# Performance work log

Hardware: AMD Instinct MI355X
Metric: run time of the kernel (lower is better)

## Reference

```python
import jax, jax.numpy as jnp
import numpy as np

DIM = 1024
HEADS = 16
DH = DIM // HEADS          # 64
ROT_DIM = 2 * DH           # 128, rotary applied over concatenated x/a head dim
B, N = 2, 2048


def l2norm(t, eps=1e-12):
    # F.normalize(p=2, dim=-1)
    n = jnp.sqrt(jnp.sum(t * t, axis=-1, keepdims=True))
    return t / jnp.maximum(n, eps)


def rotate_half(t):
    t1, t2 = jnp.split(t, 2, axis=-1)
    return jnp.concatenate([-t2, t1], axis=-1)


def apply_rotary(q, k):
    # q: [b,h,n,ROT_DIM], k: [b,1,n,ROT_DIM]
    n = q.shape[-2]
    inv_freq = 1.0 / (10000.0 ** (jnp.arange(0, ROT_DIM, 2, dtype=jnp.float32) / ROT_DIM))
    freqs = jnp.outer(jnp.arange(n, dtype=jnp.float32), inv_freq)  # [n, ROT_DIM/2]
    emb = jnp.concatenate([freqs, freqs], axis=-1)                 # [n, ROT_DIM]
    cos, sin = jnp.cos(emb), jnp.sin(emb)
    q = q * cos + rotate_half(q) * sin
    k = k * cos + rotate_half(k) * sin
    return q, k


def setup_inputs() -> dict:
    key = jax.random.key(0)
    ks = jax.random.split(key, 6)
    s = 0.02
    return {
        "x": jax.random.normal(ks[0], (B, N, DIM), jnp.float32),
        "a": jax.random.normal(ks[1], (B, N, DIM), jnp.float32),
        "Wq_x": jax.random.normal(ks[2], (DIM, DIM), jnp.float32) * s,
        "Wkv_x": jax.random.normal(ks[3], (2 * DH, DIM), jnp.float32) * s,
        "Wq_a": jax.random.normal(ks[4], (DIM, DIM), jnp.float32) * s,
        "Wkv_a": jax.random.normal(ks[5], (2 * DH, DIM), jnp.float32) * s,
        "qx_scale": jnp.ones((HEADS, 1, DH), jnp.float32),
        "qa_scale": jnp.ones((HEADS, 1, DH), jnp.float32),
        "kx_scale": jnp.ones((1, 1, DH), jnp.float32),
        "ka_scale": jnp.ones((1, 1, DH), jnp.float32),
    }


def reference(x, a, Wq_x, Wkv_x, Wq_a, Wkv_a, qx_scale, qa_scale, kx_scale, ka_scale):
    b, n, _ = x.shape
    # q projections: [b,n,dim] -> [b,h,n,dh]
    q_x = (x @ Wq_x.T).reshape(b, n, HEADS, DH).transpose(0, 2, 1, 3)
    q_a = (a @ Wq_a.T).reshape(b, n, HEADS, DH).transpose(0, 2, 1, 3)
    # shared single KV head: [b,n,2*dh] -> two [b,1,n,dh]
    kv_x = x @ Wkv_x.T
    k_x, v_x = jnp.split(kv_x[:, None], 2, axis=-1)
    kv_a = a @ Wkv_a.T
    k_a, v_a = jnp.split(kv_a[:, None], 2, axis=-1)
    # qk-norm with learned per-head (q) / shared (k) scales
    q_x = l2norm(q_x) * qx_scale
    q_a = l2norm(q_a) * qa_scale
    k_x = l2norm(k_x) * kx_scale
    k_a = l2norm(k_a) * ka_scale
    # concat modalities along feature dim -> head dim 2*dh
    q = jnp.concatenate([q_x, q_a], axis=-1)   # [b,h,n,2dh]
    k = jnp.concatenate([k_x, k_a], axis=-1)   # [b,1,n,2dh]
    v = jnp.concatenate([v_x, v_a], axis=-1)   # [b,1,n,2dh]
    q, k = apply_rotary(q, k)
    # SDPA with broadcasted single KV head
    scale = 1.0 / jnp.sqrt(jnp.float32(ROT_DIM))
    k2, v2 = k[:, 0], v[:, 0]                  # [b,n,2dh]
    scores = jnp.einsum("bhqd,bkd->bhqk", q * scale, k2)
    attn = jax.nn.softmax(scores, axis=-1)
    out = jnp.einsum("bhqk,bkd->bhqd", attn, v2)  # [b,h,n,2dh]
    return out.transpose(0, 2, 1, 3).reshape(b, n, HEADS * ROT_DIM)
```

## Files before the change

### kernel.cpp

```cpp
#include <hip/hip_runtime.h>
#include <math.h>

#define DIM   1024
#define HEADS 16
#define DH    64
#define ROT   128
#define BATCH 2
#define SEQ   2048
#define ROWS  (BATCH*SEQ)
#define PCOLS (DIM + 2*DH)
#define ASCALE (0.08838834764831845f * 1.4426950408889634f)

typedef short bf16x8 __attribute__((ext_vector_type(8)));
typedef float f32x16 __attribute__((ext_vector_type(16)));
typedef unsigned u32x2 __attribute__((ext_vector_type(2)));

static __device__ __forceinline__ unsigned short f2bf(float f) {
    union { float f; unsigned u; } v; v.f = f;
    unsigned r = v.u + 0x7fffu + ((v.u >> 16) & 1u);
    return (unsigned short)(r >> 16);
}
static __device__ __forceinline__ float bf2f(unsigned short u) {
    union { unsigned u; float f; } v; v.u = (unsigned)u << 16;
    return v.f;
}

#define GL2LDS(gp, lp) __builtin_amdgcn_global_load_lds(                    \
    (const __attribute__((address_space(1))) void*)(gp),                    \
    (__attribute__((address_space(3))) void*)(lp), 16, 0, 0)
#define CFENCE() asm volatile("" ::: "memory")
#define WAIT_VM0()  __builtin_amdgcn_s_waitcnt(0xF70)

__global__ __launch_bounds__(256) void convert_kernel(
    const float* __restrict__ x, const float* __restrict__ a,
    const float* __restrict__ Wq_x, const float* __restrict__ Wkv_x,
    const float* __restrict__ Wq_a, const float* __restrict__ Wkv_a,
    unsigned short* __restrict__ xbf, unsigned short* __restrict__ wbf,
    float2* __restrict__ tbl)
{
    const int blk = blockIdx.x;
    const float LN1E4_64 = 0.14391156831213f;
    if (blk >= 2624) {
        int local = blk - 2624;
        int pos = local * 16 + (threadIdx.x >> 4);
        int i   = threadIdx.x & 15;
        #pragma unroll
        for (int j = 0; j < 4; j++) {
            int jd = i * 4 + j;
            float th = (float)pos * expf(-LN1E4_64 * (float)jd);
            float sn, cs; sincosf(th, &sn, &cs);
            tbl[pos * 64 + jd] = make_float2(cs, sn);
        }
        return;
    }
    const float* s; unsigned short* d; int seg0;
    if      (blk < 1024) { s = x;     d = xbf;           seg0 = 0;    }
    else if (blk < 2048) { s = a;     d = xbf + 4194304; seg0 = 1024; }
    else if (blk < 2304) { s = Wq_x;  d = wbf;           seg0 = 2048; }
    else if (blk < 2336) { s = Wkv_x; d = wbf + 1048576; seg0 = 2304; }
    else if (blk < 2592) { s = Wq_a;  d = wbf + 1179648; seg0 = 2336; }
    else                 { s = Wkv_a; d = wbf + 2228224; seg0 = 2592; }
    long lb = ((long)blk - seg0) * 1024;
    #pragma unroll
    for (int j = 0; j < 4; j++) {
        long idx = lb + j * 256 + threadIdx.x;
        float4 v = ((const float4*)s)[idx];
        ((ushort4*)d)[idx] = make_ushort4(f2bf(v.x), f2bf(v.y), f2bf(v.z), f2bf(v.w));
    }
}

__global__ __launch_bounds__(512) void gemm_fuse_kernel(
    const unsigned short* __restrict__ xbf, const unsigned short* __restrict__ wbf,
    const float* __restrict__ qx_scale, const float* __restrict__ qa_scale,
    const float* __restrict__ kx_scale, const float* __restrict__ ka_scale,
    const float2* __restrict__ tbl,
    unsigned short* __restrict__ qbuf, unsigned short* __restrict__ kbuf,
    unsigned short* __restrict__ vbufT)
{
    const int mt = blockIdx.x, jt = blockIdx.y;
    __shared__ __align__(16) char scg[32768];
    const int tid  = threadIdx.x;
    const int wave = tid >> 6, lane = tid & 63;
    const int m = lane & 31, hl = lane >> 5;
    const int wr = wave >> 1, wc = wave & 1;

    f32x16 acc0[2], acc1[2];
    acc0[0] = 0.0f; acc0[1] = 0.0f; acc1[0] = 0.0f; acc1[1] = 0.0f;

    const int srow = tid >> 2;
    const int sg   = (tid & 3) ^ ((srow >> 1) & 3);
    const unsigned short* Asrc = xbf + (size_t)mt * 128 * DIM + (size_t)srow * DIM + sg * 8;
    const unsigned short* Bsrc = wbf + (size_t)jt * 128 * DIM + (size_t)srow * DIM + sg * 8;
    const unsigned ldsw = (unsigned)wave * 1024;

    const int ra = wr * 32 + m;
    unsigned aoff[2], boff[2][2];
    #pragma unroll
    for (int kp = 0; kp < 2; kp++) {
        aoff[kp] = (unsigned)(ra * 64 + (((kp * 2 + hl) ^ ((ra >> 1) & 3)) << 4));
        #pragma unroll
        for (int j2 = 0; j2 < 2; j2++) {
            int rb = wc * 64 + j2 * 32 + m;
            boff[kp][j2] = (unsigned)(rb * 64 + (((kp * 2 + hl) ^ ((rb >> 1) & 3)) << 4));
        }
    }

    GL2LDS(Asrc, scg + ldsw);
    GL2LDS(Bsrc, scg + 16384 + ldsw);

#define GEMM_STEP(ACC, BUF, T)                                                   \
  {                                                                              \
    CFENCE();                                                                    \
    WAIT_VM0();                                                                  \
    __builtin_amdgcn_s_barrier();                                                \
    CFENCE();                                                                    \
    if ((T) < 63) {                                                              \
      const int nt = (T) + 1;                                                    \
      const size_t so = (size_t)(nt >> 5);                                       \
      const int kk = (nt & 31) * 32;                                             \
      GL2LDS(Asrc + so * ((size_t)ROWS * DIM) + kk,                              \
             scg + ((BUF) ^ 1) * 8192 + ldsw);                                   \
      GL2LDS(Bsrc + so * ((size_t)PCOLS * DIM) + kk,                             \
             scg + 16384 + ((BUF) ^ 1) * 8192 + ldsw);                           \
    }                                                                            \
    CFENCE();                                                                    \
    _Pragma("unroll")                                                            \
    for (int kp = 0; kp < 2; kp++) {                                             \
      bf16x8 af = *(const bf16x8*)(scg + (BUF) * 8192 + aoff[kp]);               \
      bf16x8 b0 = *(const bf16x8*)(scg + 16384 + (BUF) * 8192 + boff[kp][0]);    \
      bf16x8 b1 = *(const bf16x8*)(scg + 16384 + (BUF) * 8192 + boff[kp][1]);    \
      ACC[0] = __builtin_amdgcn_mfma_f32_32x32x16_bf16(af, b0, ACC[0], 0, 0, 0); \
      ACC[1] = __builtin_amdgcn_mfma_f32_32x32x16_bf16(af, b1, ACC[1], 0, 0, 0); \
    }                                                                            \
  }

    for (int tt = 0; tt < 32; tt += 2) { GEMM_STEP(acc0, 0, tt); GEMM_STEP(acc0, 1, tt + 1); }
    for (int tt = 32; tt < 64; tt += 2) { GEMM_STEP(acc1, 0, tt); GEMM_STEP(acc1, 1, tt + 1); }
#undef GEMM_STEP

    const int rowbase = mt * 128 + wr * 32;
    const int bb = rowbase >> 11;

    if (jt < 8) {
        const int h = jt * 2 + wc;
        const float scx0 = qx_scale[h * DH + m], scx1 = qx_scale[h * DH + 32 + m];
        const float sca0 = qa_scale[h * DH + m], sca1 = qa_scale[h * DH + 32 + m];
        unsigned short* qbase = qbuf + ((size_t)(bb * HEADS + h)) * SEQ * ROT;
        #pragma unroll
        for (int r = 0; r < 16; r++) {
            float px = acc0[0][r] * acc0[0][r] + acc0[1][r] * acc0[1][r];
            float pa = acc1[0][r] * acc1[0][r] + acc1[1][r] * acc1[1][r];
            #pragma unroll
            for (int off = 1; off < 32; off <<= 1) {
                px += __shfl_xor(px, off);
                pa += __shfl_xor(pa, off);
            }
            float inx = 1.0f / fmaxf(sqrtf(px), 1e-12f);
            float ina = 1.0f / fmaxf(sqrtf(pa), 1e-12f);
            const int row = rowbase + (r & 3) + 8 * (r >> 2) + 4 * hl;
            const int pos = row & 2047;
            const float2* tp = tbl + pos * 64;
            unsigned short* qrow = qbase + (size_t)pos * ROT;
            #pragma unroll
            for (int j2 = 0; j2 < 2; j2++) {
                const int d = j2 * 32 + m;
                float qx = acc0[j2][r] * inx * (j2 ? scx1 : scx0);
                float qa = acc1[j2][r] * ina * (j2 ? sca1 : sca0);
                float2 cs = tp[d];
                qrow[d]      = f2bf((qx * cs.x - qa * cs.y) * ASCALE);
                qrow[DH + d] = f2bf((qa * cs.x + qx * cs.y) * ASCALE);
            }
        }
    } else if (wc == 0) {
        const float scx0 = kx_scale[m], scx1 = kx_scale[32 + m];
        const float sca0 = ka_scale[m], sca1 = ka_scale[32 + m];
        unsigned short* kbase = kbuf + (size_t)bb * SEQ * ROT;
        #pragma unroll
        for (int r = 0; r < 16; r++) {
            float px = acc0[0][r] * acc0[0][r] + acc0[1][r] * acc0[1][r];
            float pa = acc1[0][r] * acc1[0][r] + acc1[1][r] * acc1[1][r];
            #pragma unroll
            for (int off = 1; off < 32; off <<= 1) {
                px += __shfl_xor(px, off);
                pa += __shfl_xor(pa, off);
            }
            float inx = 1.0f / fmaxf(sqrtf(px), 1e-12f);
            float ina = 1.0f / fmaxf(sqrtf(pa), 1e-12f);
            const int row = rowbase + (r & 3) + 8 * (r >> 2) + 4 * hl;
            const int pos = row & 2047;
            const float2* tp = tbl + pos * 64;
            unsigned short* krow = kbase + (size_t)pos * ROT;
            #pragma unroll
            for (int j2 = 0; j2 < 2; j2++) {
                const int d = j2 * 32 + m;
                float kx = acc0[j2][r] * inx * (j2 ? scx1 : scx0);
                float ka = acc1[j2][r] * ina * (j2 ? sca1 : sca0);
                float2 cs = tp[d];
                krow[d]      = f2bf(kx * cs.x - ka * cs.y);
                krow[DH + d] = f2bf(ka * cs.x + kx * cs.y);
            }
        }
    } else {
        unsigned short* vb = vbufT + (size_t)bb * ROT * SEQ;
        #pragma unroll
        for (int r = 0; r < 16; r++) {
            const int row = rowbase + (r & 3) + 8 * (r >> 2) + 4 * hl;
            const int pos = row & 2047;
            #pragma unroll
            for (int j2 = 0; j2 < 2; j2++) {
                const int d = j2 * 32 + m;
                vb[(size_t)d * SEQ + pos]        = f2bf(acc0[j2][r]);
                vb[(size_t)(DH + d) * SEQ + pos] = f2bf(acc1[j2][r]);
            }
        }
    }
}

__global__ __launch_bounds__(256, 2) void attn_kernel(
    const unsigned short* __restrict__ qbuf,
    const unsigned short* __restrict__ kbuf,
    const unsigned short* __restrict__ vbufT,
    float* __restrict__ out)
{
    const int qb = blockIdx.x, h = blockIdx.y, b = blockIdx.z;
    __shared__ __align__(16) unsigned short smem[32768];
    const char* sc = (const char*)smem;
    const int tid  = threadIdx.x;
    const int wave = tid >> 6, lane = tid & 63;
    const int m = lane & 31, hl = lane >> 5;
    const int q0 = qb * 128 + wave * 32;

    bf16x8 qf[8];
    {
        const unsigned short* qp = qbuf + (((size_t)(b * HEADS + h)) * SEQ + q0 + m) * ROT + hl * 8;
        #pragma unroll
        for (int c = 0; c < 8; c++) qf[c] = *(const bf16x8*)(qp + c * 16);
    }

    f32x16 oacc[4];
    #pragma unroll
    for (int dt = 0; dt < 4; dt++) oacc[dt] = 0.0f;
    float lsum = 0.f;

    unsigned koff[8];
    #pragma unroll
    for (int c = 0; c < 8; c++)
        koff[c] = (unsigned)(m * 256 + (((2 * c + hl) ^ (m & 15)) << 4));
    unsigned voff[2][2];
    #pragma unroll
    for (int kg = 0; kg < 2; kg++)
        #pragma unroll
        for (int w = 0; w < 2; w++)
            voff[kg][w] = (unsigned)(32768 + m * 128 +
                                     (((kg * 4 + w * 2 + hl) ^ ((m >> 2) & 7)) << 4));

    const unsigned short* kb_ = kbuf  + (size_t)b * SEQ * ROT;
    const unsigned short* vb_ = vbufT + (size_t)b * ROT * SEQ;

    const unsigned short* ksrc[4];
    const unsigned short* vsrc[4];
    unsigned ldst[4];
    #pragma unroll
    for (int i = 0; i < 4; i++) {
        int fg = i * 256 + tid;
        int krow = fg >> 4, kgr = fg & 15;
        ksrc[i] = kb_ + (size_t)krow * ROT + ((kgr ^ (krow & 15)) << 3);
        int rv = fg >> 3, gv = fg & 7;
        vsrc[i] = vb_ + (size_t)rv * SEQ + ((gv ^ ((rv >> 2) & 7)) << 3);
        ldst[i] = (unsigned)(i * 256 + wave * 64) * 16;
    }

    #pragma unroll
    for (int i = 0; i < 4; i++) {
        GL2LDS(ksrc[i], sc + ldst[i]);
        GL2LDS(vsrc[i], sc + 32768 + ldst[i]);
    }

#define ATTN_TILE(BUF, T)                                                            \
  {                                                                                  \
    CFENCE();                                                                        \
    WAIT_VM0();                                                                      \
    __builtin_amdgcn_s_barrier();                                                    \
    CFENCE();                                                                        \
    if ((T) < 31) {                          \
      _Pragma("unroll")                                                              \
      for (int i = 0; i < 4; i++) {                                                  \
        GL2LDS(ksrc[i] + (size_t)((T) + 1) * 64 * ROT,                               \
               sc + ((BUF) ^ 1) * 16384 + ldst[i]);                                  \
        GL2LDS(vsrc[i] + ((T) + 1) * 64,                                             \
               sc + 32768 + ((BUF) ^ 1) * 16384 + ldst[i]);                          \
      }                                                                              \
    }                                                                                \
    CFENCE();                                                                        \
    f32x16 st0 = 0.0f, st1 = 0.0f;                                                   \
    __builtin_amdgcn_s_setprio(1);                                                   \
    _Pragma("unroll")                                                                \
    for (int c = 0; c < 8; c++) {                                                    \
      bf16x8 a0 = *(const bf16x8*)(sc + (BUF) * 16384 + koff[c]);                    \
      st0 = __builtin_amdgcn_mfma_f32_32x32x16_bf16(a0, qf[c], st0, 0, 0, 0);        \
    }                                                                                \
    _Pragma("unroll")                                                                \
    for (int c = 0; c < 8; c++) {                                                    \
      bf16x8 a1 = *(const bf16x8*)(sc + (BUF) * 16384 + 8192 + koff[c]);             \
      st1 = __builtin_amdgcn_mfma_f32_32x32x16_bf16(a1, qf[c], st1, 0, 0, 0);        \
    }                                                                                \
    __builtin_amdgcn_s_setprio(0);                                                   \
    _Pragma("unroll")                                                                \
    for (int kg = 0; kg < 2; kg++) {                                                 \
      float p[16];                                                                   \
      _Pragma("unroll")                                                              \
      for (int r = 0; r < 16; r++) {                                                 \
        float sv = kg ? st1[r] : st0[r];                                             \
        p[r] = __builtin_amdgcn_exp2f(sv); lsum += p[r];                             \
      }                                                                              \
      __builtin_amdgcn_s_setprio(1);                                                 \
      _Pragma("unroll")                                                              \
      for (int w = 0; w < 2; w++) {                                                  \
        unsigned pk0, pk1, pk2, pk3;                                                 \
        asm("v_cvt_pk_bf16_f32 %0, %1, %2" : "=v"(pk0) : "v"(p[8*w+0]), "v"(p[8*w+1])); \
        asm("v_cvt_pk_bf16_f32 %0, %1, %2" : "=v"(pk1) : "v"(p[8*w+2]), "v"(p[8*w+3])); \
        asm("v_cvt_pk_bf16_f32 %0, %1, %2" : "=v"(pk2) : "v"(p[8*w+4]), "v"(p[8*w+5])); \
        asm("v_cvt_pk_bf16_f32 %0, %1, %2" : "=v"(pk3) : "v"(p[8*w+6]), "v"(p[8*w+7])); \
        u32x2 s0 = __builtin_amdgcn_permlane32_swap(pk0, pk2, false, false);         \
        u32x2 s1 = __builtin_amdgcn_permlane32_swap(pk1, pk3, false, false);         \
        union { unsigned u[4]; bf16x8 v; } apu;                                      \
        apu.u[0] = s0[0]; apu.u[1] = s1[0]; apu.u[2] = s0[1]; apu.u[3] = s1[1];      \
        bf16x8 aP = apu.v;                                                           \
        _Pragma("unroll")                                                            \
        for (int dt = 0; dt < 4; dt++) {                                             \
          bf16x8 vf = *(const bf16x8*)(sc + (BUF) * 16384 + voff[kg][w] + dt * 4096);\
          oacc[dt] = __builtin_amdgcn_mfma_f32_32x32x16_bf16(aP, vf, oacc[dt], 0, 0, 0); \
        }                                                                            \
      }                                                                              \
      __builtin_amdgcn_s_setprio(0);                                                 \
    }                                                                                \
  }

    for (int tt = 0; tt < 32; tt += 2) {
        ATTN_TILE(0, tt);
        ATTN_TILE(1, tt + 1);
    }
#undef ATTN_TILE

    lsum += __shfl_xor(lsum, 32);
    float* ob = out + ((size_t)(b * SEQ + q0)) * (HEADS * ROT) + h * ROT + m;
    #pragma unroll
    for (int r = 0; r < 16; r++) {
        int qrow = (r & 3) + 8 * (r >> 2) + 4 * hl;
        float linv = 1.0f / __shfl(lsum, qrow);
        float* orow = ob + (size_t)qrow * (HEADS * ROT);
        #pragma unroll
        for (int dt = 0; dt < 4; dt++) orow[dt * 32] = oacc[dt][r] * linv;
    }
}

extern "C" void kernel_launch(void* const* d_in, const int* in_sizes, int n_in,
                              void* d_out, int out_size, void* d_ws, size_t ws_size,
                              hipStream_t stream) {
    (void)in_sizes; (void)n_in; (void)out_size; (void)ws_size;
    const float* x        = (const float*)d_in[0];
    const float* a        = (const float*)d_in[1];
    const float* Wq_x     = (const float*)d_in[2];
    const float* Wkv_x    = (const float*)d_in[3];
    const float* Wq_a     = (const float*)d_in[4];
    const float* Wkv_a    = (const float*)d_in[5];
    const float* qx_scale = (const float*)d_in[6];
    const float* qa_scale = (const float*)d_in[7];
    const float* kx_scale = (const float*)d_in[8];
    const float* ka_scale = (const float*)d_in[9];
    float* out = (float*)d_out;

    unsigned short* Pbf   = (unsigned short*)d_ws;
    unsigned short* qbuf  = Pbf   + (size_t)2 * ROWS * PCOLS;
    unsigned short* kbuf  = qbuf  + (size_t)BATCH * HEADS * SEQ * ROT;
    unsigned short* vbufT = kbuf  + (size_t)BATCH * SEQ * ROT;
    unsigned short* xbf   = vbufT + (size_t)BATCH * SEQ * ROT;
    unsigned short* wbf   = xbf   + (size_t)2 * ROWS * DIM;
    float2*         tbl   = (float2*)(wbf + (size_t)2 * PCOLS * DIM);

    convert_kernel<<<dim3(2752), 256, 0, stream>>>(x, a, Wq_x, Wkv_x, Wq_a, Wkv_a,
                                                   xbf, wbf, tbl);
    gemm_fuse_kernel<<<dim3(32, 9), 512, 0, stream>>>(xbf, wbf,
                                                      qx_scale, qa_scale, kx_scale, ka_scale,
                                                      tbl, qbuf, kbuf, vbufT);
    attn_kernel<<<dim3(SEQ / 128, HEADS, BATCH), 256, 0, stream>>>(qbuf, kbuf, vbufT, out);
}
```

Before: 217.0 us.

## Split attention over KV halves, shrink GEMM tiles, and add merge kernel

The projection GEMM moves from 512-thread blocks with 128x128 tiles to 256-thread blocks with 64x128 tiles, which doubles the grid and lowers LDS per block. Attention now splits the key sequence into two halves across extra grid blocks and uses 32-key tiles with a single score accumulator. Each half writes unnormalized partial outputs and row sums, and a new merge kernel adds the halves and normalizes. This adds occupancy and parallelism at the cost of an extra kernel launch and extra global traffic for the partial outputs. Merging by plain summation with no max correction depends on the scores being bounded, which holds because q and k are l2-normalized.

After: 291.0 us. 34.1% more time.

```diff
diff --git a/kernel.cpp b/kernel.cpp
--- a/kernel.cpp
+++ b/kernel.cpp
@@ -69,7 +69,7 @@
     }
 }
 
-__global__ __launch_bounds__(512) void gemm_fuse_kernel(
+__global__ __launch_bounds__(256, 4) void gemm_fuse_kernel(
     const unsigned short* __restrict__ xbf, const unsigned short* __restrict__ wbf,
     const float* __restrict__ qx_scale, const float* __restrict__ qa_scale,
     const float* __restrict__ kx_scale, const float* __restrict__ ka_scale,
@@ -78,7 +78,7 @@
     unsigned short* __restrict__ vbufT)
 {
     const int mt = blockIdx.x, jt = blockIdx.y;
-    __shared__ __align__(16) char scg[32768];
+    __shared__ __align__(16) char scg[24576];
     const int tid  = threadIdx.x;
     const int wave = tid >> 6, lane = tid & 63;
     const int m = lane & 31, hl = lane >> 5;
@@ -87,11 +87,18 @@
     f32x16 acc0[2], acc1[2];
     acc0[0] = 0.0f; acc0[1] = 0.0f; acc1[0] = 0.0f; acc1[1] = 0.0f;
 
-    const int srow = tid >> 2;
-    const int sg   = (tid & 3) ^ ((srow >> 1) & 3);
-    const unsigned short* Asrc = xbf + (size_t)mt * 128 * DIM + (size_t)srow * DIM + sg * 8;
-    const unsigned short* Bsrc = wbf + (size_t)jt * 128 * DIM + (size_t)srow * DIM + sg * 8;
-    const unsigned ldsw = (unsigned)wave * 1024;
+    const int arow = tid >> 2;
+    const int ag   = (tid & 3) ^ ((arow >> 1) & 3);
+    const unsigned short* Asrc = xbf + ((size_t)mt * 64 + arow) * DIM + ag * 8;
+    const unsigned short* Bsrc[2];
+    #pragma unroll
+    for (int i = 0; i < 2; i++) {
+        int fg = i * 256 + tid;
+        int brow = fg >> 2;
+        int bg = (fg & 3) ^ ((brow >> 1) & 3);
+        Bsrc[i] = wbf + ((size_t)jt * 128 + brow) * DIM + bg * 8;
+    }
+    const unsigned adst = (unsigned)wave * 1024;
 
     const int ra = wr * 32 + m;
     unsigned aoff[2], boff[2][2];
@@ -105,8 +112,9 @@
         }
     }
 
-    GL2LDS(Asrc, scg + ldsw);
-    GL2LDS(Bsrc, scg + 16384 + ldsw);
+    GL2LDS(Asrc, scg + adst);
+    GL2LDS(Bsrc[0], scg + 8192 + adst);
+    GL2LDS(Bsrc[1], scg + 8192 + 4096 + adst);
 
 #define GEMM_STEP(ACC, BUF, T)                                                   \
   {                                                                              \
@@ -119,16 +127,18 @@
       const size_t so = (size_t)(nt >> 5);                                       \
       const int kk = (nt & 31) * 32;                                             \
       GL2LDS(Asrc + so * ((size_t)ROWS * DIM) + kk,                              \
-             scg + ((BUF) ^ 1) * 8192 + ldsw);                                   \
-      GL2LDS(Bsrc + so * ((size_t)PCOLS * DIM) + kk,                             \
-             scg + 16384 + ((BUF) ^ 1) * 8192 + ldsw);                           \
+             scg + ((BUF) ^ 1) * 4096 + adst);                                   \
+      GL2LDS(Bsrc[0] + so * ((size_t)PCOLS * DIM) + kk,                          \
+             scg + 8192 + ((BUF) ^ 1) * 8192 + adst);                            \
+      GL2LDS(Bsrc[1] + so * ((size_t)PCOLS * DIM) + kk,                          \
+             scg + 8192 + ((BUF) ^ 1) * 8192 + 4096 + adst);                     \
     }                                                                            \
     CFENCE();                                                                    \
     _Pragma("unroll")                                                            \
     for (int kp = 0; kp < 2; kp++) {                                             \
-      bf16x8 af = *(const bf16x8*)(scg + (BUF) * 8192 + aoff[kp]);               \
-      bf16x8 b0 = *(const bf16x8*)(scg + 16384 + (BUF) * 8192 + boff[kp][0]);    \
-      bf16x8 b1 = *(const bf16x8*)(scg + 16384 + (BUF) * 8192 + boff[kp][1]);    \
+      bf16x8 af = *(const bf16x8*)(scg + (BUF) * 4096 + aoff[kp]);               \
+      bf16x8 b0 = *(const bf16x8*)(scg + 8192 + (BUF) * 8192 + boff[kp][0]);     \
+      bf16x8 b1 = *(const bf16x8*)(scg + 8192 + (BUF) * 8192 + boff[kp][1]);     \
       ACC[0] = __builtin_amdgcn_mfma_f32_32x32x16_bf16(af, b0, ACC[0], 0, 0, 0); \
       ACC[1] = __builtin_amdgcn_mfma_f32_32x32x16_bf16(af, b1, ACC[1], 0, 0, 0); \
     }                                                                            \
@@ -138,7 +148,7 @@
     for (int tt = 32; tt < 64; tt += 2) { GEMM_STEP(acc1, 0, tt); GEMM_STEP(acc1, 1, tt + 1); }
 #undef GEMM_STEP
 
-    const int rowbase = mt * 128 + wr * 32;
+    const int rowbase = mt * 64 + wr * 32;
     const int bb = rowbase >> 11;
 
     if (jt < 8) {
@@ -216,15 +226,16 @@
     }
 }
 
-__global__ __launch_bounds__(256, 2) void attn_kernel(
+__global__ __launch_bounds__(256, 4) void attn_kernel(
     const unsigned short* __restrict__ qbuf,
     const unsigned short* __restrict__ kbuf,
     const unsigned short* __restrict__ vbufT,
-    float* __restrict__ out)
+    float* __restrict__ po0, float* __restrict__ po1, float* __restrict__ pl)
 {
-    const int qb = blockIdx.x, h = blockIdx.y, b = blockIdx.z;
-    __shared__ __align__(16) unsigned short smem[32768];
-    const char* sc = (const char*)smem;
+    const int qb = blockIdx.x, h = blockIdx.y;
+    const int b = blockIdx.z & 1, s = blockIdx.z >> 1;
+    __shared__ __align__(16) char sc_[32768];
+    const char* sc = sc_;
     const int tid  = threadIdx.x;
     const int wave = tid >> 6, lane = tid & 63;
     const int m = lane & 31, hl = lane >> 5;
@@ -246,34 +257,31 @@
     #pragma unroll
     for (int c = 0; c < 8; c++)
         koff[c] = (unsigned)(m * 256 + (((2 * c + hl) ^ (m & 15)) << 4));
-    unsigned voff[2][2];
-    #pragma unroll
-    for (int kg = 0; kg < 2; kg++)
-        #pragma unroll
-        for (int w = 0; w < 2; w++)
-            voff[kg][w] = (unsigned)(32768 + m * 128 +
-                                     (((kg * 4 + w * 2 + hl) ^ ((m >> 2) & 7)) << 4));
-
-    const unsigned short* kb_ = kbuf  + (size_t)b * SEQ * ROT;
-    const unsigned short* vb_ = vbufT + (size_t)b * ROT * SEQ;
-
-    const unsigned short* ksrc[4];
-    const unsigned short* vsrc[4];
-    unsigned ldst[4];
-    #pragma unroll
-    for (int i = 0; i < 4; i++) {
+    unsigned voff[2];
+    #pragma unroll
+    for (int w = 0; w < 2; w++)
+        voff[w] = (unsigned)(16384 + m * 64 + (((w * 2 + hl) ^ ((m >> 2) & 3)) << 4));
+
+    const unsigned short* kb_ = kbuf  + (size_t)b * SEQ * ROT + (size_t)s * 1024 * ROT;
+    const unsigned short* vb_ = vbufT + (size_t)b * ROT * SEQ + (size_t)s * 1024;
+
+    const unsigned short* ksrc[2];
+    const unsigned short* vsrc[2];
+    unsigned ldst[2];
+    #pragma unroll
+    for (int i = 0; i < 2; i++) {
         int fg = i * 256 + tid;
         int krow = fg >> 4, kgr = fg & 15;
         ksrc[i] = kb_ + (size_t)krow * ROT + ((kgr ^ (krow & 15)) << 3);
-        int rv = fg >> 3, gv = fg & 7;
-        vsrc[i] = vb_ + (size_t)rv * SEQ + ((gv ^ ((rv >> 2) & 7)) << 3);
-        ldst[i] = (unsigned)(i * 256 + wave * 64) * 16;
-    }
-
-    #pragma unroll
-    for (int i = 0; i < 4; i++) {
+        int rv = fg >> 2, gv = fg & 3;
+        vsrc[i] = vb_ + (size_t)rv * SEQ + ((gv ^ ((rv >> 2) & 3)) << 3);
+        ldst[i] = (unsigned)(i * 4096 + wave * 1024);
+    }
+
+    #pragma unroll
+    for (int i = 0; i < 2; i++) {
         GL2LDS(ksrc[i], sc + ldst[i]);
-        GL2LDS(vsrc[i], sc + 32768 + ldst[i]);
+        GL2LDS(vsrc[i], sc + 16384 + ldst[i]);
     }
 
 #define ATTN_TILE(BUF, T)                                                            \
@@ -284,53 +292,42 @@
     CFENCE();                                                                        \
     if ((T) < 31) {                          \
       _Pragma("unroll")                                                              \
-      for (int i = 0; i < 4; i++) {                                                  \
-        GL2LDS(ksrc[i] + (size_t)((T) + 1) * 64 * ROT,                               \
-               sc + ((BUF) ^ 1) * 16384 + ldst[i]);                                  \
-        GL2LDS(vsrc[i] + ((T) + 1) * 64,                                             \
-               sc + 32768 + ((BUF) ^ 1) * 16384 + ldst[i]);                          \
+      for (int i = 0; i < 2; i++) {                                                  \
+        GL2LDS(ksrc[i] + (size_t)((T) + 1) * 32 * ROT,                               \
+               sc + ((BUF) ^ 1) * 8192 + ldst[i]);                                   \
+        GL2LDS(vsrc[i] + (size_t)((T) + 1) * 32,                                     \
+               sc + 16384 + ((BUF) ^ 1) * 8192 + ldst[i]);                           \
       }                                                                              \
     }                                                                                \
     CFENCE();                                                                        \
-    f32x16 st0 = 0.0f, st1 = 0.0f;                                                   \
+    f32x16 st = 0.0f;                                                                \
     __builtin_amdgcn_s_setprio(1);                                                   \
     _Pragma("unroll")                                                                \
     for (int c = 0; c < 8; c++) {                                                    \
-      bf16x8 a0 = *(const bf16x8*)(sc + (BUF) * 16384 + koff[c]);                    \
-      st0 = __builtin_amdgcn_mfma_f32_32x32x16_bf16(a0, qf[c], st0, 0, 0, 0);        \
-    }                                                                                \
-    _Pragma("unroll")                                                                \
-    for (int c = 0; c < 8; c++) {                                                    \
-      bf16x8 a1 = *(const bf16x8*)(sc + (BUF) * 16384 + 8192 + koff[c]);             \
-      st1 = __builtin_amdgcn_mfma_f32_32x32x16_bf16(a1, qf[c], st1, 0, 0, 0);        \
+      bf16x8 a0 = *(const bf16x8*)(sc + (BUF) * 8192 + koff[c]);                     \
+      st = __builtin_amdgcn_mfma_f32_32x32x16_bf16(a0, qf[c], st, 0, 0, 0);          \
     }                                                                                \
     __builtin_amdgcn_s_setprio(0);                                                   \
+    float p[16];                                                                     \
     _Pragma("unroll")                                                                \
-    for (int kg = 0; kg < 2; kg++) {                                                 \
-      float p[16];                                                                   \
-      _Pragma("unroll")                                                              \
-      for (int r = 0; r < 16; r++) {                                                 \
-        float sv = kg ? st1[r] : st0[r];                                             \
-        p[r] = __builtin_amdgcn_exp2f(sv); lsum += p[r];                             \
-      }                                                                              \
+    for (int r = 0; r < 16; r++) { p[r] = __builtin_amdgcn_exp2f(st[r]); lsum += p[r]; } \
+    _Pragma("unroll")                                                                \
+    for (int w = 0; w < 2; w++) {                                                    \
+      unsigned pk0, pk1, pk2, pk3;                                                   \
+      asm("v_cvt_pk_bf16_f32 %0, %1, %2" : "=v"(pk0) : "v"(p[8*w+0]), "v"(p[8*w+1])); \
+      asm("v_cvt_pk_bf16_f32 %0, %1, %2" : "=v"(pk1) : "v"(p[8*w+2]), "v"(p[8*w+3])); \
+      asm("v_cvt_pk_bf16_f32 %0, %1, %2" : "=v"(pk2) : "v"(p[8*w+4]), "v"(p[8*w+5])); \
+      asm("v_cvt_pk_bf16_f32 %0, %1, %2" : "=v"(pk3) : "v"(p[8*w+6]), "v"(p[8*w+7])); \
+      u32x2 s0 = __builtin_amdgcn_permlane32_swap(pk0, pk2, false, false);           \
+      u32x2 s1 = __builtin_amdgcn_permlane32_swap(pk1, pk3, false, false);           \
+      union { unsigned u[4]; bf16x8 v; } apu;                                        \
+      apu.u[0] = s0[0]; apu.u[1] = s1[0]; apu.u[2] = s0[1]; apu.u[3] = s1[1];        \
+      bf16x8 aP = apu.v;                                                             \
       __builtin_amdgcn_s_setprio(1);                                                 \
       _Pragma("unroll")                                                              \
-      for (int w = 0; w < 2; w++) {                                                  \
-        unsigned pk0, pk1, pk2, pk3;                                                 \
-        asm("v_cvt_pk_bf16_f32 %0, %1, %2" : "=v"(pk0) : "v"(p[8*w+0]), "v"(p[8*w+1])); \
-        asm("v_cvt_pk_bf16_f32 %0, %1, %2" : "=v"(pk1) : "v"(p[8*w+2]), "v"(p[8*w+3])); \
-        asm("v_cvt_pk_bf16_f32 %0, %1, %2" : "=v"(pk2) : "v"(p[8*w+4]), "v"(p[8*w+5])); \
-        asm("v_cvt_pk_bf16_f32 %0, %1, %2" : "=v"(pk3) : "v"(p[8*w+6]), "v"(p[8*w+7])); \
-        u32x2 s0 = __builtin_amdgcn_permlane32_swap(pk0, pk2, false, false);         \
-        u32x2 s1 = __builtin_amdgcn_permlane32_swap(pk1, pk3, false, false);         \
-        union { unsigned u[4]; bf16x8 v; } apu;                                      \
-        apu.u[0] = s0[0]; apu.u[1] = s1[0]; apu.u[2] = s0[1]; apu.u[3] = s1[1];      \
-        bf16x8 aP = apu.v;                                                           \
-        _Pragma("unroll")                                                            \
-        for (int dt = 0; dt < 4; dt++) {                                             \
-          bf16x8 vf = *(const bf16x8*)(sc + (BUF) * 16384 + voff[kg][w] + dt * 4096);\
-          oacc[dt] = __builtin_amdgcn_mfma_f32_32x32x16_bf16(aP, vf, oacc[dt], 0, 0, 0); \
-        }                                                                            \
+      for (int dt = 0; dt < 4; dt++) {                                               \
+        bf16x8 vf = *(const bf16x8*)(sc + (BUF) * 8192 + voff[w] + dt * 2048);       \
+        oacc[dt] = __builtin_amdgcn_mfma_f32_32x32x16_bf16(aP, vf, oacc[dt], 0, 0, 0); \
       }                                                                              \
       __builtin_amdgcn_s_setprio(0);                                                 \
     }                                                                                \
@@ -343,14 +340,44 @@
 #undef ATTN_TILE
 
     lsum += __shfl_xor(lsum, 32);
-    float* ob = out + ((size_t)(b * SEQ + q0)) * (HEADS * ROT) + h * ROT + m;
+    float* pbase = s ? po1 : po0;
+    float* ob = pbase + ((size_t)(b * SEQ + q0)) * (HEADS * ROT) + h * ROT + m;
     #pragma unroll
     for (int r = 0; r < 16; r++) {
         int qrow = (r & 3) + 8 * (r >> 2) + 4 * hl;
-        float linv = 1.0f / __shfl(lsum, qrow);
         float* orow = ob + (size_t)qrow * (HEADS * ROT);
         #pragma unroll
-        for (int dt = 0; dt < 4; dt++) orow[dt * 32] = oacc[dt][r] * linv;
+        for (int dt = 0; dt < 4; dt++) orow[dt * 32] = oacc[dt][r];
+    }
+    if (lane < 32)
+        pl[(((size_t)s * BATCH + b) * HEADS + h) * SEQ + q0 + m] = lsum;
+}
+
+__global__ __launch_bounds__(256) void merge_kernel(
+    float* __restrict__ out, const float* __restrict__ po1,
+    const float* __restrict__ pl)
+{
+    const int tid = threadIdx.x;
+    const size_t base = (size_t)blockIdx.x * 1024 + tid;
+    #pragma unroll
+    for (int j = 0; j < 4; j++) {
+        size_t fi = base + (size_t)j * 256;
+        size_t ei = fi * 4;
+        int b   = (int)(ei >> 22);
+        int rem = (int)(ei & 4194303);
+        int pos = rem >> 11;
+        int h   = (rem >> 7) & 15;
+        float l0 = pl[((size_t)(b)*HEADS + h) * SEQ + pos];
+        float l1 = pl[((size_t)(2 + b) * HEADS + h) * SEQ + pos];
+        float inv = 1.0f / (l0 + l1);
+        float4 o0 = ((const float4*)out)[fi];
+        float4 o1 = ((const float4*)po1)[fi];
+        float4 r;
+        r.x = (o0.x + o1.x) * inv;
+        r.y = (o0.y + o1.y) * inv;
+        r.z = (o0.z + o1.z) * inv;
+        r.w = (o0.w + o1.w) * inv;
+        ((float4*)out)[fi] = r;
     }
 }
 
@@ -370,18 +397,22 @@
     const float* ka_scale = (const float*)d_in[9];
     float* out = (float*)d_out;
 
-    unsigned short* Pbf   = (unsigned short*)d_ws;
-    unsigned short* qbuf  = Pbf   + (size_t)2 * ROWS * PCOLS;
-    unsigned short* kbuf  = qbuf  + (size_t)BATCH * HEADS * SEQ * ROT;
-    unsigned short* vbufT = kbuf  + (size_t)BATCH * SEQ * ROT;
-    unsigned short* xbf   = vbufT + (size_t)BATCH * SEQ * ROT;
-    unsigned short* wbf   = xbf   + (size_t)2 * ROWS * DIM;
-    float2*         tbl   = (float2*)(wbf + (size_t)2 * PCOLS * DIM);
+    char* ws = (char*)d_ws;
+    unsigned short* qbuf  = (unsigned short*)(ws);
+    unsigned short* kbuf  = (unsigned short*)(ws + 16777216);
+    unsigned short* vbufT = (unsigned short*)(ws + 17825792);
+    float*          pl    = (float*)(ws + 18874368);
+    unsigned short* xbf   = (unsigned short*)(ws + 19398656);
+    unsigned short* wbf   = (unsigned short*)(ws + 36175872);
+    float2*         tbl   = (float2*)(ws + 40894464);
+    float*          po1   = (float*)(ws + 19398656);
 
     convert_kernel<<<dim3(2752), 256, 0, stream>>>(x, a, Wq_x, Wkv_x, Wq_a, Wkv_a,
                                                    xbf, wbf, tbl);
-    gemm_fuse_kernel<<<dim3(32, 9), 512, 0, stream>>>(xbf, wbf,
+    gemm_fuse_kernel<<<dim3(64, 9), 256, 0, stream>>>(xbf, wbf,
                                                       qx_scale, qa_scale, kx_scale, ka_scale,
                                                       tbl, qbuf, kbuf, vbufT);
-    attn_kernel<<<dim3(SEQ / 128, HEADS, BATCH), 256, 0, stream>>>(qbuf, kbuf, vbufT, out);
-}
+    attn_kernel<<<dim3(SEQ / 128, HEADS, 2 * BATCH), 256, 0, stream>>>(qbuf, kbuf, vbufT,
+                                                                       out, po1, pl);
+    merge_kernel<<<dim3(2048), 256, 0, stream>>>(out, po1, pl);
+}
```

## Halve GEMM M-tile and deepen LDS pipeline to four stages

Applied to the files above, without the earlier changes.

The projection GEMM now uses 256-thread blocks computing 64x128 tiles, doubling the grid from 288 to 576 blocks so more of the CUs are filled. The LDS ring grows to four stages with a two-step prefetch distance, and the wait drops from waiting on all loads to a partial vmcnt, so global-to-LDS loads overlap MFMA work for longer. The cost is a larger LDS footprint per block, more B-tile reloads because the M tile is smaller, and more delicate vmcnt accounting. The workspace offsets are also rewritten as fixed byte offsets, dropping the unused Pbf region.

Result: slower. 223.1 us (+2.8%).

```diff
diff --git a/kernel.cpp b/kernel.cpp
--- a/kernel.cpp
+++ b/kernel.cpp
@@ -29,6 +29,7 @@
     (const __attribute__((address_space(1))) void*)(gp),                    \
     (__attribute__((address_space(3))) void*)(lp), 16, 0, 0)
 #define CFENCE() asm volatile("" ::: "memory")
+#define WAIT_VM3()  __builtin_amdgcn_s_waitcnt(0xF73)
 #define WAIT_VM0()  __builtin_amdgcn_s_waitcnt(0xF70)
 
 __global__ __launch_bounds__(256) void convert_kernel(
@@ -69,7 +70,7 @@
     }
 }
 
-__global__ __launch_bounds__(512) void gemm_fuse_kernel(
+__global__ __launch_bounds__(256, 3) void gemm_fuse_kernel(
     const unsigned short* __restrict__ xbf, const unsigned short* __restrict__ wbf,
     const float* __restrict__ qx_scale, const float* __restrict__ qa_scale,
     const float* __restrict__ kx_scale, const float* __restrict__ ka_scale,
@@ -78,7 +79,7 @@
     unsigned short* __restrict__ vbufT)
 {
     const int mt = blockIdx.x, jt = blockIdx.y;
-    __shared__ __align__(16) char scg[32768];
+    __shared__ __align__(16) char scg[49152];
     const int tid  = threadIdx.x;
     const int wave = tid >> 6, lane = tid & 63;
     const int m = lane & 31, hl = lane >> 5;
@@ -87,11 +88,18 @@
     f32x16 acc0[2], acc1[2];
     acc0[0] = 0.0f; acc0[1] = 0.0f; acc1[0] = 0.0f; acc1[1] = 0.0f;
 
-    const int srow = tid >> 2;
-    const int sg   = (tid & 3) ^ ((srow >> 1) & 3);
-    const unsigned short* Asrc = xbf + (size_t)mt * 128 * DIM + (size_t)srow * DIM + sg * 8;
-    const unsigned short* Bsrc = wbf + (size_t)jt * 128 * DIM + (size_t)srow * DIM + sg * 8;
-    const unsigned ldsw = (unsigned)wave * 1024;
+    const int arow = tid >> 2;
+    const int ag   = (tid & 3) ^ ((arow >> 1) & 3);
+    const unsigned short* Asrc = xbf + ((size_t)mt * 64 + arow) * DIM + ag * 8;
+    const unsigned short* Bsrc[2];
+    #pragma unroll
+    for (int i = 0; i < 2; i++) {
+        int fg = i * 256 + tid;
+        int brow = fg >> 2;
+        int bg = (fg & 3) ^ ((brow >> 1) & 3);
+        Bsrc[i] = wbf + ((size_t)jt * 128 + brow) * DIM + bg * 8;
+    }
+    const unsigned adst = (unsigned)wave * 1024;
 
     const int ra = wr * 32 + m;
     unsigned aoff[2], boff[2][2];
@@ -105,28 +113,34 @@
         }
     }
 
-    GL2LDS(Asrc, scg + ldsw);
-    GL2LDS(Bsrc, scg + 16384 + ldsw);
+    GL2LDS(Asrc, scg + adst);
+    GL2LDS(Bsrc[0], scg + 16384 + adst);
+    GL2LDS(Bsrc[1], scg + 16384 + 4096 + adst);
+    GL2LDS(Asrc + 32, scg + 4096 + adst);
+    GL2LDS(Bsrc[0] + 32, scg + 16384 + 8192 + adst);
+    GL2LDS(Bsrc[1] + 32, scg + 16384 + 8192 + 4096 + adst);
 
 #define GEMM_STEP(ACC, BUF, T)                                                   \
   {                                                                              \
     CFENCE();                                                                    \
-    WAIT_VM0();                                                                  \
+    if ((T) < 63) WAIT_VM3(); else WAIT_VM0();        \
     __builtin_amdgcn_s_barrier();                                                \
     CFENCE();                                                                    \
-    if ((T) < 63) {                                                              \
-      const int nt = (T) + 1;                                                    \
+    if ((T) < 62) {                          \
+      const int nt = (T) + 2;                                                    \
       const size_t so = (size_t)(nt >> 5);                                       \
       const int kk = (nt & 31) * 32;                                             \
       GL2LDS(Asrc + so * ((size_t)ROWS * DIM) + kk,                              \
-             scg + ((BUF) ^ 1) * 8192 + ldsw);                                   \
-      GL2LDS(Bsrc + so * ((size_t)PCOLS * DIM) + kk,                             \
-             scg + 16384 + ((BUF) ^ 1) * 8192 + ldsw);                           \
+             scg + ((((T) + 2) & 3)) * 4096 + adst);                             \
+      GL2LDS(Bsrc[0] + so * ((size_t)PCOLS * DIM) + kk,                          \
+             scg + 16384 + ((((T) + 2) & 3)) * 8192 + adst);                     \
+      GL2LDS(Bsrc[1] + so * ((size_t)PCOLS * DIM) + kk,                          \
+             scg + 16384 + ((((T) + 2) & 3)) * 8192 + 4096 + adst);              \
     }                                                                            \
     CFENCE();                                                                    \
     _Pragma("unroll")                                                            \
     for (int kp = 0; kp < 2; kp++) {                                             \
-      bf16x8 af = *(const bf16x8*)(scg + (BUF) * 8192 + aoff[kp]);               \
+      bf16x8 af = *(const bf16x8*)(scg + (BUF) * 4096 + aoff[kp]);               \
       bf16x8 b0 = *(const bf16x8*)(scg + 16384 + (BUF) * 8192 + boff[kp][0]);    \
       bf16x8 b1 = *(const bf16x8*)(scg + 16384 + (BUF) * 8192 + boff[kp][1]);    \
       ACC[0] = __builtin_amdgcn_mfma_f32_32x32x16_bf16(af, b0, ACC[0], 0, 0, 0); \
@@ -134,11 +148,17 @@
     }                                                                            \
   }
 
-    for (int tt = 0; tt < 32; tt += 2) { GEMM_STEP(acc0, 0, tt); GEMM_STEP(acc0, 1, tt + 1); }
-    for (int tt = 32; tt < 64; tt += 2) { GEMM_STEP(acc1, 0, tt); GEMM_STEP(acc1, 1, tt + 1); }
+    for (int tt = 0; tt < 32; tt += 4) {
+        GEMM_STEP(acc0, 0, tt);     GEMM_STEP(acc0, 1, tt + 1);
+        GEMM_STEP(acc0, 2, tt + 2); GEMM_STEP(acc0, 3, tt + 3);
+    }
+    for (int tt = 32; tt < 64; tt += 4) {
+        GEMM_STEP(acc1, 0, tt);     GEMM_STEP(acc1, 1, tt + 1);
+        GEMM_STEP(acc1, 2, tt + 2); GEMM_STEP(acc1, 3, tt + 3);
+    }
 #undef GEMM_STEP
 
-    const int rowbase = mt * 128 + wr * 32;
+    const int rowbase = mt * 64 + wr * 32;
     const int bb = rowbase >> 11;
 
     if (jt < 8) {
@@ -370,17 +390,17 @@
     const float* ka_scale = (const float*)d_in[9];
     float* out = (float*)d_out;
 
-    unsigned short* Pbf   = (unsigned short*)d_ws;
-    unsigned short* qbuf  = Pbf   + (size_t)2 * ROWS * PCOLS;
-    unsigned short* kbuf  = qbuf  + (size_t)BATCH * HEADS * SEQ * ROT;
-    unsigned short* vbufT = kbuf  + (size_t)BATCH * SEQ * ROT;
-    unsigned short* xbf   = vbufT + (size_t)BATCH * SEQ * ROT;
-    unsigned short* wbf   = xbf   + (size_t)2 * ROWS * DIM;
-    float2*         tbl   = (float2*)(wbf + (size_t)2 * PCOLS * DIM);
+    char* ws = (char*)d_ws;
+    unsigned short* qbuf  = (unsigned short*)(ws);
+    unsigned short* kbuf  = (unsigned short*)(ws + 16777216);
+    unsigned short* vbufT = (unsigned short*)(ws + 17825792);
+    unsigned short* xbf   = (unsigned short*)(ws + 19398656);
+    unsigned short* wbf   = (unsigned short*)(ws + 36175872);
+    float2*         tbl   = (float2*)(ws + 40894464);
 
     convert_kernel<<<dim3(2752), 256, 0, stream>>>(x, a, Wq_x, Wkv_x, Wq_a, Wkv_a,
                                                    xbf, wbf, tbl);
-    gemm_fuse_kernel<<<dim3(32, 9), 512, 0, stream>>>(xbf, wbf,
+    gemm_fuse_kernel<<<dim3(64, 9), 256, 0, stream>>>(xbf, wbf,
                                                       qx_scale, qa_scale, kx_scale, ka_scale,
                                                       tbl, qbuf, kbuf, vbufT);
     attn_kernel<<<dim3(SEQ / 128, HEADS, BATCH), 256, 0, stream>>>(qbuf, kbuf, vbufT, out);
```
